# Performance work log

Measured on AMD Instinct MI355X. Metric: run time of the kernel, lower is better.

Reference implementation:

```python
import jax, jax.numpy as jnp
import numpy as np

B, N, D, L = 4, 16384, 1024, 4
NEG = -10000.0


def setup_inputs() -> dict:
    key = jax.random.key(0)
    k1, k2, k3, k4, k5 = jax.random.split(key, 5)
    xs = jax.random.normal(k1, (B, N, D), dtype=jnp.float32)
    valid = jax.random.randint(k2, (B, N), 0, 2).astype(jnp.bool_)
    # ensure at least one valid instance per bag
    valid = valid.at[:, 0].set(True)
    w1 = jax.random.normal(k3, (D, 1), dtype=jnp.float32) * (1.0 / np.sqrt(D))
    w2 = jax.random.normal(k4, (D, 1), dtype=jnp.float32) * (1.0 / np.sqrt(D))
    wf = jax.random.normal(k5, (L, D), dtype=jnp.float32) * (1.0 / np.sqrt(D))
    return {"xs": xs, "valid": valid, "w1": w1, "w2": w2, "wf": wf}


def reference(xs, valid, w1, w2, wf):
    # gated attention scores: tanh(x w1) * sigmoid(x w2)  -> [B, N]
    a = jnp.tanh(xs @ w1)[..., 0] * jax.nn.sigmoid(xs @ w2)[..., 0]
    # padding mask fill (matches a[~valid] = -10000)
    a = jnp.where(valid, a, NEG)
    att = jax.nn.softmax(a, axis=-1)            # [B, N]
    z = jnp.einsum('bn,bnd->bd', att, xs)       # weighted-sum pooling
    return z @ wf.T                              # [B, L]
```

## Files before the change

### kernel.cpp

```cpp
#include <hip/hip_runtime.h>
#include <hip/hip_bf16.h>
#include <math.h>


#define NB   4
#define NN   16384
#define DD   1024
#define LL   4
#define NBLK 256
#define RPB  (NN / NBLK)
#define RPW  (RPB / 4)

struct POut { float pd[LL]; float s; float pad[3]; };

__device__ __forceinline__ float wave_reduce(float v) {
    #pragma unroll
    for (int off = 32; off > 0; off >>= 1) v += __shfl_xor(v, off, 64);
    return v;
}

__global__ __launch_bounds__(256) void abmil_main(
    const float* __restrict__ xs, const void* __restrict__ valid,
    const float* __restrict__ w1, const float* __restrict__ w2,
    const float* __restrict__ wf, POut* __restrict__ parts) {
    const int blk  = blockIdx.x;
    const int bag  = blockIdx.y;
    const int tid  = threadIdx.x;
    const int wave = tid >> 6;
    const int lane = tid & 63;

    __shared__ int nflag[2];
    if (tid == 0) { nflag[0] = 0; nflag[1] = 0; }
    __syncthreads();
    {
        const unsigned int* vw = (const unsigned int*)valid;
        int bi = 0, bf = 0;
        #pragma unroll
        for (int j = 0; j < 4; ++j) {
            const unsigned int x = vw[tid * 4 + j];
            if (x != 0u && x != 1u) bi = 1;
            if (x != 0u && x != 0x3F800000u) bf = 1;
        }
        if (bi) atomicOr(&nflag[0], 1);
        if (bf) atomicOr(&nflag[1], 1);
    }
    __syncthreads();
    const int mode = (!nflag[0]) ? 1 : ((!nflag[1]) ? 2 : 0);

    const float4* w1v = (const float4*)w1;
    const float4* w2v = (const float4*)w2;
    float4 w1r[4], w2r[4];
    #pragma unroll
    for (int k = 0; k < 4; ++k) {
        w1r[k] = w1v[k * 64 + lane];
        w2r[k] = w2v[k * 64 + lane];
    }

    const int n0 = blk * RPB + wave * RPW;
    int flag = 0;
    if (lane < RPW) {
        const size_t idx = (size_t)bag * NN + n0 + lane;
        if (mode == 1)      flag = ((const int*)valid)[idx] != 0;
        else if (mode == 2) flag = ((const float*)valid)[idx] != 0.0f;
        else                flag = ((const unsigned char*)valid)[idx] != 0;
    }
    const unsigned long long vm = __ballot(flag);

    float s = 0.0f;
    float4 z[4];
    #pragma unroll
    for (int k = 0; k < 4; ++k) z[k] = make_float4(0.f, 0.f, 0.f, 0.f);

    const float4* xbase = (const float4*)(xs + (size_t)bag * NN * DD);

    for (int i = 0; i < RPW; i += 2) {
        const bool v0 = (vm >> i)       & 1ull;
        const bool v1 = (vm >> (i + 1)) & 1ull;
        float4 x0[4], x1[4];
        #pragma unroll
        for (int k = 0; k < 4; ++k) {
            x0[k] = make_float4(0.f, 0.f, 0.f, 0.f);
            x1[k] = make_float4(0.f, 0.f, 0.f, 0.f);
        }
        if (v0) {
            const float4* xp = xbase + (size_t)(n0 + i) * (DD / 4);
            #pragma unroll
            for (int k = 0; k < 4; ++k) x0[k] = xp[k * 64 + lane];
        }
        if (v1) {
            const float4* xp = xbase + (size_t)(n0 + i + 1) * (DD / 4);
            #pragma unroll
            for (int k = 0; k < 4; ++k) x1[k] = xp[k * 64 + lane];
        }

        float d1a = 0.f, d2a = 0.f, d1b = 0.f, d2b = 0.f;
        #pragma unroll
        for (int k = 0; k < 4; ++k) {
            d1a += x0[k].x * w1r[k].x + x0[k].y * w1r[k].y +
                   x0[k].z * w1r[k].z + x0[k].w * w1r[k].w;
            d2a += x0[k].x * w2r[k].x + x0[k].y * w2r[k].y +
                   x0[k].z * w2r[k].z + x0[k].w * w2r[k].w;
            d1b += x1[k].x * w1r[k].x + x1[k].y * w1r[k].y +
                   x1[k].z * w1r[k].z + x1[k].w * w1r[k].w;
            d2b += x1[k].x * w2r[k].x + x1[k].y * w2r[k].y +
                   x1[k].z * w2r[k].z + x1[k].w * w2r[k].w;
        }
        #pragma unroll
        for (int off = 32; off > 0; off >>= 1) {
            d1a += __shfl_xor(d1a, off, 64);
            d2a += __shfl_xor(d2a, off, 64);
            d1b += __shfl_xor(d1b, off, 64);
            d2b += __shfl_xor(d2b, off, 64);
        }
        const float a0 = tanhf(d1a) * (1.0f / (1.0f + __expf(-d2a)));
        const float a1 = tanhf(d1b) * (1.0f / (1.0f + __expf(-d2b)));
        const float p0 = v0 ? __expf(a0) : 0.0f;
        const float p1 = v1 ? __expf(a1) : 0.0f;
        s += p0 + p1;
        #pragma unroll
        for (int k = 0; k < 4; ++k) {
            z[k].x += p0 * x0[k].x + p1 * x1[k].x;
            z[k].y += p0 * x0[k].y + p1 * x1[k].y;
            z[k].z += p0 * x0[k].z + p1 * x1[k].z;
            z[k].w += p0 * x0[k].w + p1 * x1[k].w;
        }
    }

    __shared__ float zsh[4][DD];
    __shared__ float ssh[4];
    __shared__ float wsum[4][LL];
    #pragma unroll
    for (int k = 0; k < 4; ++k) ((float4*)zsh[wave])[k * 64 + lane] = z[k];
    if (lane == 0) ssh[wave] = s;
    __syncthreads();

    float pl[LL] = {0.f, 0.f, 0.f, 0.f};
    #pragma unroll
    for (int k = 0; k < 4; ++k) {
        const int d = tid + k * 256;
        const float zb = zsh[0][d] + zsh[1][d] + zsh[2][d] + zsh[3][d];
        #pragma unroll
        for (int l = 0; l < LL; ++l) pl[l] += zb * wf[l * DD + d];
    }
    #pragma unroll
    for (int l = 0; l < LL; ++l) pl[l] = wave_reduce(pl[l]);
    if (lane == 0) {
        #pragma unroll
        for (int l = 0; l < LL; ++l) wsum[wave][l] = pl[l];
    }
    __syncthreads();

    POut* po = &parts[(size_t)bag * NBLK + blk];
    if (tid < LL)
        po->pd[tid] = wsum[0][tid] + wsum[1][tid] + wsum[2][tid] + wsum[3][tid];
    if (tid == LL)
        po->s = ssh[0] + ssh[1] + ssh[2] + ssh[3];
}

__global__ __launch_bounds__(256) void abmil_finish(
    const POut* __restrict__ parts, float* __restrict__ out) {
    const int bag  = threadIdx.x >> 6;
    const int lane = threadIdx.x & 63;

    float pd[LL] = {0.f, 0.f, 0.f, 0.f};
    float s = 0.0f;
    #pragma unroll
    for (int j = 0; j < NBLK / 64; ++j) {
        const POut* p = &parts[(size_t)bag * NBLK + j * 64 + lane];
        #pragma unroll
        for (int l = 0; l < LL; ++l) pd[l] += p->pd[l];
        s += p->s;
    }
    #pragma unroll
    for (int l = 0; l < LL; ++l) pd[l] = wave_reduce(pd[l]);
    s = wave_reduce(s);
    if (lane == 0) {
        #pragma unroll
        for (int l = 0; l < LL; ++l) out[bag * LL + l] = pd[l] / s;
    }
}

extern "C" void kernel_launch(void* const* d_in, const int* in_sizes, int n_in,
                              void* d_out, int out_size, void* d_ws, size_t ws_size,
                              hipStream_t stream) {
    const float* xs    = (const float*)d_in[0];
    const void*  valid = d_in[1];
    const float* w1    = (const float*)d_in[2];
    const float* w2    = (const float*)d_in[3];
    const float* wf    = (const float*)d_in[4];
    float* out = (float*)d_out;

    POut* parts = (POut*)d_ws;

    dim3 g0(NBLK, NB);
    abmil_main<<<g0, 256, 0, stream>>>(xs, valid, w1, w2, wf, parts);
    abmil_finish<<<1, 256, 0, stream>>>(parts, out);
}
```

Before: 34.02 us.

## Iterate only valid rows with software-pipelined loads and per-wave projection

The row loop now walks only set bits of the validity mask. It uses a double-buffered prefetch, so the next valid row's load is issued before the current row is computed, and invalid rows no longer cost compute slots. tanh and sigmoid use a fast reciprocal formulation. The final projection onto wf is done per wave directly from registers, which removes the 16KB shared-memory z reduction and one barrier. Occupancy is hinted at 4 blocks per CU. The risks are small precision differences from rcp and more register pressure from the two live row buffers.

```diff
diff --git a/kernel.cpp b/kernel.cpp
--- a/kernel.cpp
+++ b/kernel.cpp
@@ -19,7 +19,18 @@
     return v;
 }
 
-__global__ __launch_bounds__(256) void abmil_main(
+__device__ __forceinline__ float fast_rcp(float x) {
+    return __builtin_amdgcn_rcpf(x);
+}
+
+__device__ __forceinline__ int popnext(unsigned& m) {
+    if (m == 0u) return -1;
+    const int i = (int)__builtin_ctz(m);
+    m &= m - 1u;
+    return i;
+}
+
+__global__ __launch_bounds__(256, 4) void abmil_main(
     const float* __restrict__ xs, const void* __restrict__ valid,
     const float* __restrict__ w1, const float* __restrict__ w2,
     const float* __restrict__ wf, POut* __restrict__ parts) {
@@ -29,17 +40,20 @@
     const int wave = tid >> 6;
     const int lane = tid & 63;
 
-    __shared__ int nflag[2];
+    __shared__ int   nflag[2];
+    __shared__ float comb[4][LL];
+    __shared__ float scomb[4];
+
     if (tid == 0) { nflag[0] = 0; nflag[1] = 0; }
     __syncthreads();
     {
-        const unsigned int* vw = (const unsigned int*)valid;
+        const uint4 xq = ((const uint4*)valid)[tid];
+        const unsigned w[4] = {xq.x, xq.y, xq.z, xq.w};
         int bi = 0, bf = 0;
         #pragma unroll
         for (int j = 0; j < 4; ++j) {
-            const unsigned int x = vw[tid * 4 + j];
-            if (x != 0u && x != 1u) bi = 1;
-            if (x != 0u && x != 0x3F800000u) bf = 1;
+            if (w[j] != 0u && w[j] != 1u) bi = 1;
+            if (w[j] != 0u && w[j] != 0x3F800000u) bf = 1;
         }
         if (bi) atomicOr(&nflag[0], 1);
         if (bf) atomicOr(&nflag[1], 1);
@@ -64,7 +78,7 @@
         else if (mode == 2) flag = ((const float*)valid)[idx] != 0.0f;
         else                flag = ((const unsigned char*)valid)[idx] != 0;
     }
-    const unsigned long long vm = __ballot(flag);
+    unsigned m = (unsigned)(__ballot(flag) & 0xFFFFull);
 
     float s = 0.0f;
     float4 z[4];
@@ -73,88 +87,74 @@
 
     const float4* xbase = (const float4*)(xs + (size_t)bag * NN * DD);
 
-    for (int i = 0; i < RPW; i += 2) {
-        const bool v0 = (vm >> i)       & 1ull;
-        const bool v1 = (vm >> (i + 1)) & 1ull;
-        float4 x0[4], x1[4];
+    auto loadrow = [&](float4 (&xr)[4], int idx) {
+        if (idx >= 0) {
+            const float4* xp = xbase + (size_t)(n0 + idx) * (DD / 4);
+            #pragma unroll
+            for (int k = 0; k < 4; ++k) xr[k] = xp[k * 64 + lane];
+        }
+    };
+    auto comprow = [&](const float4 (&xr)[4]) {
+        float d1 = 0.f, d2 = 0.f;
         #pragma unroll
         for (int k = 0; k < 4; ++k) {
-            x0[k] = make_float4(0.f, 0.f, 0.f, 0.f);
-            x1[k] = make_float4(0.f, 0.f, 0.f, 0.f);
-        }
-        if (v0) {
-            const float4* xp = xbase + (size_t)(n0 + i) * (DD / 4);
-            #pragma unroll
-            for (int k = 0; k < 4; ++k) x0[k] = xp[k * 64 + lane];
-        }
-        if (v1) {
-            const float4* xp = xbase + (size_t)(n0 + i + 1) * (DD / 4);
-            #pragma unroll
-            for (int k = 0; k < 4; ++k) x1[k] = xp[k * 64 + lane];
-        }
-
-        float d1a = 0.f, d2a = 0.f, d1b = 0.f, d2b = 0.f;
-        #pragma unroll
-        for (int k = 0; k < 4; ++k) {
-            d1a += x0[k].x * w1r[k].x + x0[k].y * w1r[k].y +
-                   x0[k].z * w1r[k].z + x0[k].w * w1r[k].w;
-            d2a += x0[k].x * w2r[k].x + x0[k].y * w2r[k].y +
-                   x0[k].z * w2r[k].z + x0[k].w * w2r[k].w;
-            d1b += x1[k].x * w1r[k].x + x1[k].y * w1r[k].y +
-                   x1[k].z * w1r[k].z + x1[k].w * w1r[k].w;
-            d2b += x1[k].x * w2r[k].x + x1[k].y * w2r[k].y +
-                   x1[k].z * w2r[k].z + x1[k].w * w2r[k].w;
+            d1 += xr[k].x * w1r[k].x + xr[k].y * w1r[k].y +
+                  xr[k].z * w1r[k].z + xr[k].w * w1r[k].w;
+            d2 += xr[k].x * w2r[k].x + xr[k].y * w2r[k].y +
+                  xr[k].z * w2r[k].z + xr[k].w * w2r[k].w;
         }
         #pragma unroll
         for (int off = 32; off > 0; off >>= 1) {
-            d1a += __shfl_xor(d1a, off, 64);
-            d2a += __shfl_xor(d2a, off, 64);
-            d1b += __shfl_xor(d1b, off, 64);
-            d2b += __shfl_xor(d2b, off, 64);
+            d1 += __shfl_xor(d1, off, 64);
+            d2 += __shfl_xor(d2, off, 64);
         }
-        const float a0 = tanhf(d1a) * (1.0f / (1.0f + __expf(-d2a)));
-        const float a1 = tanhf(d1b) * (1.0f / (1.0f + __expf(-d2b)));
-        const float p0 = v0 ? __expf(a0) : 0.0f;
-        const float p1 = v1 ? __expf(a1) : 0.0f;
-        s += p0 + p1;
+        const float e  = __expf(-2.0f * fabsf(d1));
+        const float t  = copysignf((1.0f - e) * fast_rcp(1.0f + e), d1);
+        const float sg = fast_rcp(1.0f + __expf(-d2));
+        const float p  = __expf(t * sg);
+        s += p;
         #pragma unroll
         for (int k = 0; k < 4; ++k) {
-            z[k].x += p0 * x0[k].x + p1 * x1[k].x;
-            z[k].y += p0 * x0[k].y + p1 * x1[k].y;
-            z[k].z += p0 * x0[k].z + p1 * x1[k].z;
-            z[k].w += p0 * x0[k].w + p1 * x1[k].w;
+            z[k].x += p * xr[k].x; z[k].y += p * xr[k].y;
+            z[k].z += p * xr[k].z; z[k].w += p * xr[k].w;
         }
+    };
+
+    float4 xA[4], xB[4];
+    int iA = popnext(m), iB = popnext(m);
+    loadrow(xA, iA); loadrow(xB, iB);
+    for (;;) {
+        if (iA < 0) break;
+        comprow(xA); iA = popnext(m); loadrow(xA, iA);
+        if (iB < 0) break;
+        comprow(xB); iB = popnext(m); loadrow(xB, iB);
     }
 
-    __shared__ float zsh[4][DD];
-    __shared__ float ssh[4];
-    __shared__ float wsum[4][LL];
-    #pragma unroll
-    for (int k = 0; k < 4; ++k) ((float4*)zsh[wave])[k * 64 + lane] = z[k];
-    if (lane == 0) ssh[wave] = s;
-    __syncthreads();
-
+    const float4* wfv = (const float4*)wf;
     float pl[LL] = {0.f, 0.f, 0.f, 0.f};
     #pragma unroll
-    for (int k = 0; k < 4; ++k) {
-        const int d = tid + k * 256;
-        const float zb = zsh[0][d] + zsh[1][d] + zsh[2][d] + zsh[3][d];
+    for (int l = 0; l < LL; ++l) {
         #pragma unroll
-        for (int l = 0; l < LL; ++l) pl[l] += zb * wf[l * DD + d];
+        for (int k = 0; k < 4; ++k) {
+            const float4 wv = wfv[l * 256 + k * 64 + lane];
+            pl[l] += z[k].x * wv.x + z[k].y * wv.y +
+                     z[k].z * wv.z + z[k].w * wv.w;
+        }
     }
     #pragma unroll
     for (int l = 0; l < LL; ++l) pl[l] = wave_reduce(pl[l]);
     if (lane == 0) {
         #pragma unroll
-        for (int l = 0; l < LL; ++l) wsum[wave][l] = pl[l];
+        for (int l = 0; l < LL; ++l) comb[wave][l] = pl[l];
+        scomb[wave] = s;
     }
     __syncthreads();
 
     POut* po = &parts[(size_t)bag * NBLK + blk];
     if (tid < LL)
-        po->pd[tid] = wsum[0][tid] + wsum[1][tid] + wsum[2][tid] + wsum[3][tid];
+        po->pd[tid] = comb[0][tid] + comb[1][tid] + comb[2][tid] + comb[3][tid];
     if (tid == LL)
-        po->s = ssh[0] + ssh[1] + ssh[2] + ssh[3];
+        po->s = scomb[0] + scomb[1] + scomb[2] + scomb[3];
 }
 
 __global__ __launch_bounds__(256) void abmil_finish(
```

After: 34.53 us. Within noise of the previous version (+1.5%).
